# Kernel tuning notes

Measured on AMD Instinct MI355X. Metric: run time of the kernel, lower is better.

## Reference

```python
import jax, jax.numpy as jnp
import numpy as np

N_EMB = 512
EMB_DIM = 64
COMMITMENT_COST = 0.25


def setup_inputs() -> dict:
    key = jax.random.key(0)
    k1, k2 = jax.random.split(key)
    x = jax.random.normal(k1, (32, 64, 64, EMB_DIM), dtype=jnp.float32)
    init_bound = 1.0 / N_EMB
    embedding = jax.random.uniform(k2, (N_EMB, EMB_DIM), dtype=jnp.float32,
                                   minval=-init_bound, maxval=init_bound)
    return {"x": x, "embedding": embedding}


def reference(x, embedding):
    M, D = embedding.shape
    x_flat = jax.lax.stop_gradient(x).reshape(-1, D)  # [N, D]
    # distances = (-cdist(x, E))**2 == squared euclidean distance; argmin identical
    # to argmin over cdist, computed without forming sqrt:
    d2 = (jnp.sum(x_flat * x_flat, axis=-1, keepdims=True)
          - 2.0 * (x_flat @ embedding.T)
          + jnp.sum(embedding * embedding, axis=-1))  # [N, M]
    indices = jnp.argmin(d2, axis=-1)  # [N]
    quantized = embedding[indices].reshape(x.shape)  # gather, view_as(x)

    # eval-mode (not training): commitment loss + straight-through estimator
    e_latent_loss = jnp.mean((x - jax.lax.stop_gradient(quantized)) ** 2)
    loss = COMMITMENT_COST * e_latent_loss
    quantized_st = x + jax.lax.stop_gradient(quantized - x)

    # perplexity from codebook usage (avg one-hot probabilities)
    counts = jnp.zeros((M,), dtype=jnp.float32).at[indices].add(1.0)
    avg_probs = counts / x_flat.shape[0]
    perplexity = jnp.exp(-jnp.sum(avg_probs * jnp.log(avg_probs + 1e-10)))
    return quantized_st, loss, perplexity
```

## Files before the change

### kernel.cpp

```cpp
#include <hip/hip_runtime.h>


#define D      64
#define M      512
#define N_VEC  131072
#define N_ELEM 8388608

typedef __attribute__((ext_vector_type(8))) short short8;
typedef __attribute__((ext_vector_type(4))) float f32x4;


static __device__ __forceinline__ unsigned short f2bf(float f) {
    unsigned u = __float_as_uint(f);
    return (unsigned short)((u + 0x7FFFu + ((u >> 16) & 1u)) >> 16);
}

__global__ __launch_bounds__(256)
void vq_prep(const float* __restrict__ emb, float* __restrict__ bnorm,
             unsigned short* __restrict__ planes, float* __restrict__ loss_sum) {
    const int g = blockIdx.x * 256 + threadIdx.x;
    if (g == 0) *loss_sum = 0.f;

    const int c = g >> 3, s = (g >> 2) & 1, q = g & 3;
    const float* e = emb + c * D + s * 32 + q * 8;
    short8 h;
#pragma unroll
    for (int j = 0; j < 8; ++j) h[j] = (short)f2bf(e[j]);
    const int ct = c >> 4, col = c & 15;
    *(short8*)(planes + ((ct * 2 + s) * 64 + q * 16 + col) * 8) = h;

    if ((g & 7) == 0) {
        const float* ec = emb + c * D;
        float s0 = 0.f, s1 = 0.f, s2 = 0.f, s3 = 0.f;
        for (int k = 0; k < D; k += 4) {
            float e0 = ec[k], e1 = ec[k + 1], e2 = ec[k + 2], e3 = ec[k + 3];
            s0 = fmaf(e0, e0, s0); s1 = fmaf(e1, e1, s1);
            s2 = fmaf(e2, e2, s2); s3 = fmaf(e3, e3, s3);
        }
        bnorm[c] = (s0 + s1) + (s2 + s3);
    }
}

__global__ __launch_bounds__(512, 4)
void vq_main(const float* __restrict__ x, const float* __restrict__ emb,
             const float* __restrict__ bnorm, const unsigned short* __restrict__ planes,
             float* __restrict__ out, float* __restrict__ loss_sum,
             unsigned short* __restrict__ partial) {
    __shared__ __align__(16) short sE[32768];
    __shared__ float sBn[M];
    __shared__ unsigned sCode[256];
    __shared__ unsigned sHist[M];
    __shared__ float sRed[8];

    const int tid = threadIdx.x;
    const int w = tid >> 6, lane = tid & 63;
    const int q = lane >> 4, col = lane & 15;
    const int rowBase = blockIdx.x * 256 + w * 32;

    {
        const short8* src = (const short8*)planes;
        short8* dst = (short8*)sE;
#pragma unroll
        for (int k = 0; k < 8; ++k) dst[tid + k * 512] = src[tid + k * 512];
        sBn[tid] = bnorm[tid];
        sHist[tid] = 0u;
    }

    float4 xc[8];
    {
        const float* p0 = x + (size_t)(rowBase + col) * D + q * 8;
        const float* p1 = x + (size_t)(rowBase + 16 + col) * D + q * 8;
        xc[0] = *(const float4*)(p0);      xc[1] = *(const float4*)(p0 + 4);
        xc[2] = *(const float4*)(p0 + 32); xc[3] = *(const float4*)(p0 + 36);
        xc[4] = *(const float4*)(p1);      xc[5] = *(const float4*)(p1 + 4);
        xc[6] = *(const float4*)(p1 + 32); xc[7] = *(const float4*)(p1 + 36);
    }

    float An[2];
#pragma unroll
    for (int p = 0; p < 2; ++p) {
        float4 a = xc[p * 4 + 0], b = xc[p * 4 + 1], c = xc[p * 4 + 2], d = xc[p * 4 + 3];
        float pa = (a.x * a.x + a.y * a.y) + (a.z * a.z + a.w * a.w);
        float pb = (b.x * b.x + b.y * b.y) + (b.z * b.z + b.w * b.w);
        float pc = (c.x * c.x + c.y * c.y) + (c.z * c.z + c.w * c.w);
        float pd = (d.x * d.x + d.y * d.y) + (d.z * d.z + d.w * d.w);
        float u = pa + pb, v = pc + pd;
        u += __shfl_xor(u, 16, 64); u += __shfl_xor(u, 32, 64);
        v += __shfl_xor(v, 16, 64); v += __shfl_xor(v, 32, 64);
        An[p] = u + v;
    }

    short8 XH[2][2];
#pragma unroll
    for (int p = 0; p < 2; ++p) {
        float f[16] = {xc[p*4+0].x, xc[p*4+0].y, xc[p*4+0].z, xc[p*4+0].w,
                       xc[p*4+1].x, xc[p*4+1].y, xc[p*4+1].z, xc[p*4+1].w,
                       xc[p*4+2].x, xc[p*4+2].y, xc[p*4+2].z, xc[p*4+2].w,
                       xc[p*4+3].x, xc[p*4+3].y, xc[p*4+3].z, xc[p*4+3].w};
#pragma unroll
        for (int j = 0; j < 8; ++j) {
            XH[p][0][j] = (short)f2bf(f[j]);
            XH[p][1][j] = (short)f2bf(f[8 + j]);
        }
    }

    __syncthreads();

    float best0 = 3.4e38f, best1 = 3.4e38f;
    int   bi0 = 0, bi1 = 0;
#pragma unroll 4
    for (int t = 0; t < 32; ++t) {
        const int fb = t * 1024 + lane * 8;
        short8 Eh0 = *(const short8*)&sE[fb];
        short8 Eh1 = *(const short8*)&sE[fb + 512];
        f32x4 Bn4 = *(const f32x4*)&sBn[t * 16 + q * 4];

        f32x4 a1 = {0.f, 0.f, 0.f, 0.f};
        a1 = __builtin_amdgcn_mfma_f32_16x16x32_bf16(Eh0, XH[0][0], a1, 0, 0, 0);
        a1 = __builtin_amdgcn_mfma_f32_16x16x32_bf16(Eh1, XH[0][1], a1, 0, 0, 0);
        f32x4 b1 = {0.f, 0.f, 0.f, 0.f};
        b1 = __builtin_amdgcn_mfma_f32_16x16x32_bf16(Eh0, XH[1][0], b1, 0, 0, 0);
        b1 = __builtin_amdgcn_mfma_f32_16x16x32_bf16(Eh1, XH[1][1], b1, 0, 0, 0);

#pragma unroll
        for (int r = 0; r < 4; ++r) {
            const int code = t * 16 + q * 4 + r;
            float sc0 = fmaf(-2.0f, a1[r], An[0]) + Bn4[r];
            if (sc0 < best0) { best0 = sc0; bi0 = code; }
            float sc1 = fmaf(-2.0f, b1[r], An[1]) + Bn4[r];
            if (sc1 < best1) { best1 = sc1; bi1 = code; }
        }
    }

    unsigned long long pk0 = ((unsigned long long)__float_as_uint(best0) << 32) | (unsigned)bi0;
    unsigned long long pk1 = ((unsigned long long)__float_as_uint(best1) << 32) | (unsigned)bi1;
    {
        unsigned long long o;
        o = __shfl_xor(pk0, 16, 64); if (o < pk0) pk0 = o;
        o = __shfl_xor(pk0, 32, 64); if (o < pk0) pk0 = o;
        o = __shfl_xor(pk1, 16, 64); if (o < pk1) pk1 = o;
        o = __shfl_xor(pk1, 32, 64); if (o < pk1) pk1 = o;
    }
    if (q == 0) {
        const unsigned c0 = (unsigned)pk0, c1 = (unsigned)pk1;
        sCode[w * 32 + col] = c0;
        sCode[w * 32 + 16 + col] = c1;
        atomicAdd(&sHist[c0], 1u);
        atomicAdd(&sHist[c1], 1u);
    }

    float lacc = 0.f;
#pragma unroll 2
    for (int i = 0; i < 8; ++i) {
        const int rr = i * 4 + q;
        const unsigned code = sCode[w * 32 + rr];
        const size_t a = (size_t)(rowBase + rr) * D + col * 4;
        const float4 xv = *(const float4*)(x + a);
        const float4 qv = *(const float4*)(emb + (size_t)code * D + col * 4);
        const float e0 = xv.x - qv.x, e1 = xv.y - qv.y, e2 = xv.z - qv.z, e3 = xv.w - qv.w;
        lacc = fmaf(e0, e0, lacc); lacc = fmaf(e1, e1, lacc);
        lacc = fmaf(e2, e2, lacc); lacc = fmaf(e3, e3, lacc);
        float4 o;
        o.x = xv.x - e0; o.y = xv.y - e1; o.z = xv.z - e2; o.w = xv.w - e3;
        *(float4*)(out + a) = o;
    }
#pragma unroll
    for (int off = 32; off > 0; off >>= 1) lacc += __shfl_down(lacc, off, 64);
    if (lane == 0) sRed[w] = lacc;
    __syncthreads();

    partial[(size_t)blockIdx.x * M + tid] = (unsigned short)sHist[tid];
    if (tid == 0) {
        float s = ((sRed[0] + sRed[1]) + (sRed[2] + sRed[3]))
                + ((sRed[4] + sRed[5]) + (sRed[6] + sRed[7]));
        atomicAdd(loss_sum, s);
    }
}

__global__ __launch_bounds__(512)
void vq_final(const unsigned short* __restrict__ partial,
              const float* __restrict__ loss_sum, float* __restrict__ out) {
    __shared__ unsigned sP[8][512];
    __shared__ float sRed[8];
    const int t = threadIdx.x;
    const int o = t & 63;
    const int c = t >> 6;

    unsigned acc[8] = {0, 0, 0, 0, 0, 0, 0, 0};
#pragma unroll 8
    for (int b = c * 64; b < c * 64 + 64; ++b) {
        const uint4 v = *(const uint4*)(partial + (size_t)b * M + o * 8);
        acc[0] += v.x & 0xFFFFu; acc[1] += v.x >> 16;
        acc[2] += v.y & 0xFFFFu; acc[3] += v.y >> 16;
        acc[4] += v.z & 0xFFFFu; acc[5] += v.z >> 16;
        acc[6] += v.w & 0xFFFFu; acc[7] += v.w >> 16;
    }
#pragma unroll
    for (int j = 0; j < 8; ++j) sP[c][o * 8 + j] = acc[j];
    __syncthreads();

    unsigned cnt = 0;
#pragma unroll
    for (int cc = 0; cc < 8; ++cc) cnt += sP[cc][t];
    const float p = (float)cnt * (1.0f / 131072.0f);
    float term = p * logf(p + 1e-10f);
#pragma unroll
    for (int off = 32; off > 0; off >>= 1) term += __shfl_down(term, off, 64);
    if ((t & 63) == 0) sRed[t >> 6] = term;
    __syncthreads();
    if (t == 0) {
        float s = 0.f;
#pragma unroll
        for (int w = 0; w < 8; ++w) s += sRed[w];
        out[N_ELEM]     = 0.25f * (loss_sum[0] * (1.0f / 8388608.0f));
        out[N_ELEM + 1] = expf(-s);
    }
}

extern "C" void kernel_launch(void* const* d_in, const int* in_sizes, int n_in,
                              void* d_out, int out_size, void* d_ws, size_t ws_size,
                              hipStream_t stream) {
    (void)in_sizes; (void)n_in; (void)out_size; (void)ws_size;
    const float* x   = (const float*)d_in[0];
    const float* emb = (const float*)d_in[1];
    float* out = (float*)d_out;

    float*          loss  = (float*)d_ws;
    float*          bnorm = (float*)((char*)d_ws + 64);
    unsigned short* plns  = (unsigned short*)((char*)d_ws + 4096);
    unsigned short* part  = (unsigned short*)((char*)d_ws + 131072);

    vq_prep<<<dim3(16), dim3(256), 0, stream>>>(emb, bnorm, plns, loss);
    vq_main<<<dim3(512), dim3(512), 0, stream>>>(x, emb, bnorm, plns, out, loss, part);
    vq_final<<<dim3(1), dim3(512), 0, stream>>>(part, loss, out);
}
```

Measured before the change: 108.7 us.

## Fuse final reduction into main kernel and pack argmin into 32-bit keys

Removes the separate final kernel: each block atomically adds its nonzero histogram bins into a global histogram, and the last block, found through a ticket counter, computes perplexity and loss. The argmin drops the per-row x-norm term and packs a truncated score with the code index into one 32-bit key, replacing the 64-bit shuffles and compares. Codebook norms are offset by 1.0 so scores stay positive and the unsigned compare is valid. Truncating the low 9 mantissa bits can change which code wins on near-ties, and global atomics plus the ticket add contention in exchange for one fewer launch.

```diff
diff --git a/kernel.cpp b/kernel.cpp
--- a/kernel.cpp
+++ b/kernel.cpp
@@ -17,9 +17,11 @@
 
 __global__ __launch_bounds__(256)
 void vq_prep(const float* __restrict__ emb, float* __restrict__ bnorm,
-             unsigned short* __restrict__ planes, float* __restrict__ loss_sum) {
+             unsigned short* __restrict__ planes, float* __restrict__ loss_sum,
+             unsigned* __restrict__ ticket, unsigned* __restrict__ ghist) {
     const int g = blockIdx.x * 256 + threadIdx.x;
-    if (g == 0) *loss_sum = 0.f;
+    if (g == 0) { *loss_sum = 0.f; *ticket = 0u; }
+    if (g < M) ghist[g] = 0u;
 
     const int c = g >> 3, s = (g >> 2) & 1, q = g & 3;
     const float* e = emb + c * D + s * 32 + q * 8;
@@ -37,7 +39,7 @@
             s0 = fmaf(e0, e0, s0); s1 = fmaf(e1, e1, s1);
             s2 = fmaf(e2, e2, s2); s3 = fmaf(e3, e3, s3);
         }
-        bnorm[c] = (s0 + s1) + (s2 + s3);
+        bnorm[c] = 1.0f + ((s0 + s1) + (s2 + s3));
     }
 }
 
@@ -45,12 +47,13 @@
 void vq_main(const float* __restrict__ x, const float* __restrict__ emb,
              const float* __restrict__ bnorm, const unsigned short* __restrict__ planes,
              float* __restrict__ out, float* __restrict__ loss_sum,
-             unsigned short* __restrict__ partial) {
+             unsigned* __restrict__ ticket, unsigned* __restrict__ ghist) {
     __shared__ __align__(16) short sE[32768];
     __shared__ float sBn[M];
     __shared__ unsigned sCode[256];
     __shared__ unsigned sHist[M];
     __shared__ float sRed[8];
+    __shared__ unsigned sLast;
 
     const int tid = threadIdx.x;
     const int w = tid >> 6, lane = tid & 63;
@@ -76,20 +79,6 @@
         xc[6] = *(const float4*)(p1 + 32); xc[7] = *(const float4*)(p1 + 36);
     }
 
-    float An[2];
-#pragma unroll
-    for (int p = 0; p < 2; ++p) {
-        float4 a = xc[p * 4 + 0], b = xc[p * 4 + 1], c = xc[p * 4 + 2], d = xc[p * 4 + 3];
-        float pa = (a.x * a.x + a.y * a.y) + (a.z * a.z + a.w * a.w);
-        float pb = (b.x * b.x + b.y * b.y) + (b.z * b.z + b.w * b.w);
-        float pc = (c.x * c.x + c.y * c.y) + (c.z * c.z + c.w * c.w);
-        float pd = (d.x * d.x + d.y * d.y) + (d.z * d.z + d.w * d.w);
-        float u = pa + pb, v = pc + pd;
-        u += __shfl_xor(u, 16, 64); u += __shfl_xor(u, 32, 64);
-        v += __shfl_xor(v, 16, 64); v += __shfl_xor(v, 32, 64);
-        An[p] = u + v;
-    }
-
     short8 XH[2][2];
 #pragma unroll
     for (int p = 0; p < 2; ++p) {
@@ -106,8 +95,7 @@
 
     __syncthreads();
 
-    float best0 = 3.4e38f, best1 = 3.4e38f;
-    int   bi0 = 0, bi1 = 0;
+    unsigned best0 = 0xFFFFFFFFu, best1 = 0xFFFFFFFFu;
 #pragma unroll 4
     for (int t = 0; t < 32; ++t) {
         const int fb = t * 1024 + lane * 8;
@@ -122,27 +110,27 @@
         b1 = __builtin_amdgcn_mfma_f32_16x16x32_bf16(Eh0, XH[1][0], b1, 0, 0, 0);
         b1 = __builtin_amdgcn_mfma_f32_16x16x32_bf16(Eh1, XH[1][1], b1, 0, 0, 0);
 
+        const int cb = t * 16 + q * 4;
 #pragma unroll
         for (int r = 0; r < 4; ++r) {
-            const int code = t * 16 + q * 4 + r;
-            float sc0 = fmaf(-2.0f, a1[r], An[0]) + Bn4[r];
-            if (sc0 < best0) { best0 = sc0; bi0 = code; }
-            float sc1 = fmaf(-2.0f, b1[r], An[1]) + Bn4[r];
-            if (sc1 < best1) { best1 = sc1; bi1 = code; }
-        }
-    }
-
-    unsigned long long pk0 = ((unsigned long long)__float_as_uint(best0) << 32) | (unsigned)bi0;
-    unsigned long long pk1 = ((unsigned long long)__float_as_uint(best1) << 32) | (unsigned)bi1;
-    {
-        unsigned long long o;
-        o = __shfl_xor(pk0, 16, 64); if (o < pk0) pk0 = o;
-        o = __shfl_xor(pk0, 32, 64); if (o < pk0) pk0 = o;
-        o = __shfl_xor(pk1, 16, 64); if (o < pk1) pk1 = o;
-        o = __shfl_xor(pk1, 32, 64); if (o < pk1) pk1 = o;
+            float sc0 = fmaf(-2.0f, a1[r], Bn4[r]);
+            float sc1 = fmaf(-2.0f, b1[r], Bn4[r]);
+            unsigned p0 = (__float_as_uint(sc0) & 0xFFFFFE00u) | (unsigned)(cb + r);
+            unsigned p1 = (__float_as_uint(sc1) & 0xFFFFFE00u) | (unsigned)(cb + r);
+            best0 = p0 < best0 ? p0 : best0;
+            best1 = p1 < best1 ? p1 : best1;
+        }
+    }
+
+    {
+        unsigned o;
+        o = __shfl_xor(best0, 16, 64); best0 = o < best0 ? o : best0;
+        o = __shfl_xor(best0, 32, 64); best0 = o < best0 ? o : best0;
+        o = __shfl_xor(best1, 16, 64); best1 = o < best1 ? o : best1;
+        o = __shfl_xor(best1, 32, 64); best1 = o < best1 ? o : best1;
     }
     if (q == 0) {
-        const unsigned c0 = (unsigned)pk0, c1 = (unsigned)pk1;
+        const unsigned c0 = best0 & 511u, c1 = best1 & 511u;
         sCode[w * 32 + col] = c0;
         sCode[w * 32 + 16 + col] = c1;
         atomicAdd(&sHist[c0], 1u);
@@ -169,51 +157,39 @@
     if (lane == 0) sRed[w] = lacc;
     __syncthreads();
 
-    partial[(size_t)blockIdx.x * M + tid] = (unsigned short)sHist[tid];
+    {
+        const unsigned h = sHist[tid];
+        if (h) atomicAdd(&ghist[tid], h);
+    }
     if (tid == 0) {
         float s = ((sRed[0] + sRed[1]) + (sRed[2] + sRed[3]))
                 + ((sRed[4] + sRed[5]) + (sRed[6] + sRed[7]));
         atomicAdd(loss_sum, s);
     }
-}
-
-__global__ __launch_bounds__(512)
-void vq_final(const unsigned short* __restrict__ partial,
-              const float* __restrict__ loss_sum, float* __restrict__ out) {
-    __shared__ unsigned sP[8][512];
-    __shared__ float sRed[8];
-    const int t = threadIdx.x;
-    const int o = t & 63;
-    const int c = t >> 6;
-
-    unsigned acc[8] = {0, 0, 0, 0, 0, 0, 0, 0};
-#pragma unroll 8
-    for (int b = c * 64; b < c * 64 + 64; ++b) {
-        const uint4 v = *(const uint4*)(partial + (size_t)b * M + o * 8);
-        acc[0] += v.x & 0xFFFFu; acc[1] += v.x >> 16;
-        acc[2] += v.y & 0xFFFFu; acc[3] += v.y >> 16;
-        acc[4] += v.z & 0xFFFFu; acc[5] += v.z >> 16;
-        acc[6] += v.w & 0xFFFFu; acc[7] += v.w >> 16;
-    }
-#pragma unroll
-    for (int j = 0; j < 8; ++j) sP[c][o * 8 + j] = acc[j];
-    __syncthreads();
-
-    unsigned cnt = 0;
-#pragma unroll
-    for (int cc = 0; cc < 8; ++cc) cnt += sP[cc][t];
-    const float p = (float)cnt * (1.0f / 131072.0f);
-    float term = p * logf(p + 1e-10f);
-#pragma unroll
-    for (int off = 32; off > 0; off >>= 1) term += __shfl_down(term, off, 64);
-    if ((t & 63) == 0) sRed[t >> 6] = term;
-    __syncthreads();
-    if (t == 0) {
-        float s = 0.f;
-#pragma unroll
-        for (int w = 0; w < 8; ++w) s += sRed[w];
-        out[N_ELEM]     = 0.25f * (loss_sum[0] * (1.0f / 8388608.0f));
-        out[N_ELEM + 1] = expf(-s);
+    __syncthreads();
+
+    if (tid == 0) {
+        __threadfence();
+        sLast = (atomicAdd(ticket, 1u) == 511u) ? 1u : 0u;
+    }
+    __syncthreads();
+
+    if (sLast) {
+        const unsigned cnt = atomicAdd(&ghist[tid], 0u);
+        const float p = (float)cnt * (1.0f / 131072.0f);
+        float term = p * logf(p + 1e-10f);
+#pragma unroll
+        for (int off = 32; off > 0; off >>= 1) term += __shfl_down(term, off, 64);
+        if (lane == 0) sRed[w] = term;
+        __syncthreads();
+        if (tid == 0) {
+            float s = 0.f;
+#pragma unroll
+            for (int ww = 0; ww < 8; ++ww) s += sRed[ww];
+            const float L = atomicAdd(loss_sum, 0.0f);
+            out[N_ELEM]     = 0.25f * (L * (1.0f / 8388608.0f));
+            out[N_ELEM + 1] = expf(-s);
+        }
     }
 }
 
@@ -225,12 +201,13 @@
     const float* emb = (const float*)d_in[1];
     float* out = (float*)d_out;
 
-    float*          loss  = (float*)d_ws;
-    float*          bnorm = (float*)((char*)d_ws + 64);
-    unsigned short* plns  = (unsigned short*)((char*)d_ws + 4096);
-    unsigned short* part  = (unsigned short*)((char*)d_ws + 131072);
-
-    vq_prep<<<dim3(16), dim3(256), 0, stream>>>(emb, bnorm, plns, loss);
-    vq_main<<<dim3(512), dim3(512), 0, stream>>>(x, emb, bnorm, plns, out, loss, part);
-    vq_final<<<dim3(1), dim3(512), 0, stream>>>(part, loss, out);
-}
+    float*          loss   = (float*)d_ws;
+    unsigned*       ticket = (unsigned*)((char*)d_ws + 32);
+    float*          bnorm  = (float*)((char*)d_ws + 64);
+    unsigned short* plns   = (unsigned short*)((char*)d_ws + 4096);
+    unsigned*       ghist  = (unsigned*)((char*)d_ws + 131072);
+
+    vq_prep<<<dim3(16), dim3(256), 0, stream>>>(emb, bnorm, plns, loss, ticket, ghist);
+    vq_main<<<dim3(512), dim3(512), 0, stream>>>(x, emb, bnorm, plns, out, loss,
+                                                 ticket, ghist);
+}
```

Measured after the change: 113.4 us. 1.04x slower.
